# Performance work log

Measured on AMD Instinct MI355X. Metric: run time of the kernel, lower is better.

The kernel has to match this reference:

```python
import jax, jax.numpy as jnp
import numpy as np

COMPRESSION = 2  # max-pool factor along flattened spatial axis for phi and g


def setup_inputs() -> dict:
    key = jax.random.key(0)
    ks = jax.random.split(key, 5)
    B, C, H, W = 4, 64, 96, 96
    Ci = 32  # intermediate_dim = C // 2
    s = 1.0 / np.sqrt(C)
    return {
        "x": jax.random.normal(ks[0], (B, C, H, W), dtype=jnp.float32),
        "w_theta": jax.random.normal(ks[1], (Ci, C), dtype=jnp.float32) * s,
        "b_theta": jnp.zeros((Ci,), dtype=jnp.float32),
        "w_phi": jax.random.normal(ks[2], (Ci, C), dtype=jnp.float32) * s,
        "b_phi": jnp.zeros((Ci,), dtype=jnp.float32),
        "w_g": jax.random.normal(ks[3], (Ci, C), dtype=jnp.float32) * s,
        "b_g": jnp.zeros((Ci,), dtype=jnp.float32),
        "w_out": jax.random.normal(ks[4], (C, Ci), dtype=jnp.float32) * (1.0 / np.sqrt(Ci)),
        "b_out": jnp.zeros((C,), dtype=jnp.float32),
    }


def reference(x, w_theta, b_theta, w_phi, b_phi, w_g, b_g, w_out, b_out):
    B, C, H, W = x.shape
    N = H * W
    xf = x.reshape(B, C, N).transpose(0, 2, 1)            # [B, N, C]
    # 1x1 conv projections == channel matmuls
    theta = xf @ w_theta.T + b_theta                      # [B, N, Ci]
    phi = xf @ w_phi.T + b_phi                            # [B, N, Ci]
    g = xf @ w_g.T + b_g                                  # [B, N, Ci]
    # compression: max-pool (kernel=stride=COMPRESSION) along flattened spatial axis
    Ci = theta.shape[-1]
    phi = phi.reshape(B, N // COMPRESSION, COMPRESSION, Ci).max(axis=2)  # [B, N/c, Ci]
    g = g.reshape(B, N // COMPRESSION, COMPRESSION, Ci).max(axis=2)      # [B, N/c, Ci]
    # embedded-gaussian affinity + softmax
    attn = jax.nn.softmax(jnp.einsum('bnc,bmc->bnm', theta, phi), axis=-1)  # [B, N, N/c]
    y = jnp.einsum('bnm,bmc->bnc', attn, g)               # [B, N, Ci]
    out = y @ w_out.T + b_out                             # [B, N, C]
    out = out.transpose(0, 2, 1).reshape(B, C, H, W)
    return out + x  # residual
```

## Files before the change

### kernel.cpp

```cpp
#include <hip/hip_runtime.h>
#include <hip/hip_bf16.h>


#define NQ 9216
#define MM 4608
#define LOG2E 1.44269504088896340736f

typedef __attribute__((ext_vector_type(8))) short bf16x8;
typedef __attribute__((ext_vector_type(4))) float f32x4;
typedef __attribute__((ext_vector_type(4))) unsigned short u16x4;

static __device__ __forceinline__ unsigned pk2(float a, float b) {
    __hip_bfloat162 h = __float22bfloat162_rn(make_float2(a, b));
    return *reinterpret_cast<unsigned*>(&h);
}

__global__ __launch_bounds__(128, 4) void proj_kernel(
    const float* __restrict__ x,
    const float* __restrict__ wt, const float* __restrict__ bt,
    const float* __restrict__ wp, const float* __restrict__ bp,
    const float* __restrict__ wg, const float* __restrict__ bg,
    unsigned short* __restrict__ theta, unsigned short* __restrict__ phi,
    unsigned short* __restrict__ gT, float* __restrict__ pzero)
{
    __shared__ unsigned short gst[32 * 20];

    const int tid  = threadIdx.x;
    const int wid  = tid >> 6;
    const int lane = tid & 63;
    const int q = lane >> 4;
    const int c = lane & 15;

    {
        const int gs = gridDim.x * blockDim.x;
        float4 z4 = {0.f, 0.f, 0.f, 0.f};
        for (int i = blockIdx.x * blockDim.x + tid; i < 304128; i += gs)
            ((float4*)pzero)[i] = z4;
    }

    const int b     = blockIdx.x / 288;
    const int rem   = blockIdx.x % 288;
    const int n0blk = rem * 32;
    const int n0    = n0blk + wid * 16;

    const float* Wm[3] = {wt, wp, wg};
    const float* Bm[3] = {bt, bp, bg};

    bf16x8 wf[3][2][2];
    float bias[3][2];
#pragma unroll
    for (int p = 0; p < 3; ++p) {
#pragma unroll
        for (int ct = 0; ct < 2; ++ct) {
            bias[p][ct] = Bm[p][ct * 16 + c];
#pragma unroll
            for (int ks = 0; ks < 2; ++ks) {
                const float* wsrc = Wm[p] + (ct * 16 + c) * 64 + ks * 32 + q * 8;
                f32x4 w0 = *(const f32x4*)wsrc;
                f32x4 w1 = *(const f32x4*)(wsrc + 4);
                unsigned* wk = (unsigned*)&wf[p][ct][ks];
                wk[0] = pk2(w0[0], w0[1]); wk[1] = pk2(w0[2], w0[3]);
                wk[2] = pk2(w1[0], w1[1]); wk[3] = pk2(w1[2], w1[3]);
            }
        }
    }

    bf16x8 af[2];
#pragma unroll
    for (int ks = 0; ks < 2; ++ks) {
        unsigned* ap = (unsigned*)&af[ks];
#pragma unroll
        for (int j2 = 0; j2 < 4; ++j2) {
            float x0 = x[(b * 64 + ks * 32 + q * 8 + j2 * 2) * NQ + n0 + c];
            float x1 = x[(b * 64 + ks * 32 + q * 8 + j2 * 2 + 1) * NQ + n0 + c];
            ap[j2] = pk2(x0, x1);
        }
    }

#pragma unroll
    for (int p = 0; p < 3; ++p) {
#pragma unroll
        for (int ct = 0; ct < 2; ++ct) {
            f32x4 acc = {0.f, 0.f, 0.f, 0.f};
            acc = __builtin_amdgcn_mfma_f32_16x16x32_bf16(af[0], wf[p][ct][0], acc, 0, 0, 0);
            acc = __builtin_amdgcn_mfma_f32_16x16x32_bf16(af[1], wf[p][ct][1], acc, 0, 0, 0);
#pragma unroll
            for (int r = 0; r < 4; ++r) acc[r] += bias[p][ct];
            const int ci = ct * 16 + c;
            if (p == 0) {
                unsigned pv0 = pk2(acc[0] * LOG2E, acc[1] * LOG2E);
                unsigned pv1 = pk2(acc[2] * LOG2E, acc[3] * LOG2E);
                theta[(b * NQ + n0 + 4 * q + 0) * 32 + ci] = (unsigned short)pv0;
                theta[(b * NQ + n0 + 4 * q + 1) * 32 + ci] = (unsigned short)(pv0 >> 16);
                theta[(b * NQ + n0 + 4 * q + 2) * 32 + ci] = (unsigned short)pv1;
                theta[(b * NQ + n0 + 4 * q + 3) * 32 + ci] = (unsigned short)(pv1 >> 16);
            } else {
                unsigned pv = pk2(fmaxf(acc[0], acc[1]), fmaxf(acc[2], acc[3]));
                if (p == 1) {
                    const int m0 = (n0 >> 1) + 2 * q;
                    phi[(b * MM + m0) * 32 + ci]     = (unsigned short)pv;
                    phi[(b * MM + m0 + 1) * 32 + ci] = (unsigned short)(pv >> 16);
                } else {
                    *(unsigned int*)(gst + ci * 20 + wid * 8 + 2 * q) = pv;
                }
            }
        }
    }

    __syncthreads();
    {
        const int ci = tid >> 2;
        const int m4 = (tid & 3) * 4;
        u16x4 v = *(const u16x4*)(gst + ci * 20 + m4);
        *(u16x4*)(gT + (b * 32 + ci) * MM + rem * 16 + m4) = v;
    }
}

__global__ __launch_bounds__(128, 3) void attn_kernel(
    const unsigned short* __restrict__ theta, const unsigned short* __restrict__ phi,
    const unsigned short* __restrict__ gT,
    float* __restrict__ pacc, float* __restrict__ plsum)
{
    __shared__ unsigned short pld[2][64 * 64];

    const int tid  = threadIdx.x;
    const int w    = tid >> 6;
    const int lane = tid & 63;
    const int q  = lane >> 4;
    const int c  = lane & 15;
    const int xr = (c & 7) << 3;

    const int ks  = blockIdx.x / 288;
    const int rem = blockIdx.x % 288;
    const int b   = rem / 72;
    const int nb  = (rem % 72) * 128 + w * 64;

    bf16x8 qf[4];
#pragma unroll
    for (int rt = 0; rt < 4; ++rt)
        qf[rt] = *(const bf16x8*)(theta + (b * NQ + nb + rt * 16 + c) * 32 + q * 8);

    bf16x8 onef;
    {
        unsigned v = (c == 0) ? 0x3F803F80u : 0u;
        unsigned* op = (unsigned*)&onef;
        op[0] = v; op[1] = v; op[2] = v; op[3] = v;
    }

    const unsigned short* phiB = phi + (size_t)b * MM * 32;
    const unsigned short* gTB  = gT + (size_t)b * 32 * MM;
    unsigned short* myp = pld[w];

    f32x4 acc[4][2];
    f32x4 lacc[4];
#pragma unroll
    for (int rt = 0; rt < 4; ++rt) {
        lacc[rt] = (f32x4){0.f, 0.f, 0.f, 0.f};
#pragma unroll
        for (int s2 = 0; s2 < 2; ++s2) acc[rt][s2] = (f32x4){0.f, 0.f, 0.f, 0.f};
    }

    const int mt0 = ks * 9;
    bf16x8 kf[4], vf[2][2];

#define LOAD_KF(m0) do {                                                      \
    _Pragma("unroll")                                                         \
    for (int mct = 0; mct < 4; ++mct)                                         \
        kf[mct] = *(const bf16x8*)(phiB + ((m0) + mct * 16 + c) * 32 + q * 8);\
} while (0)

#define LOAD_VF(m0) do {                                                      \
    _Pragma("unroll")                                                         \
    for (int s2 = 0; s2 < 2; ++s2) {                                          \
        _Pragma("unroll")                                                     \
        for (int st = 0; st < 2; ++st)                                        \
            vf[s2][st] = *(const bf16x8*)(gTB + (s2 * 16 + c) * MM + (m0) + st * 32 + q * 8); \
    }                                                                         \
} while (0)

#define S_STEP(rt) do {                                                       \
    _Pragma("unroll")                                                         \
    for (int mct = 0; mct < 4; ++mct) {                                       \
        f32x4 z = {0.f, 0.f, 0.f, 0.f};                                       \
        f32x4 s = __builtin_amdgcn_mfma_f32_16x16x32_bf16(kf[mct], qf[rt], z, 0, 0, 0); \
        uint2 hv = {pk2(__builtin_amdgcn_exp2f(s[0]), __builtin_amdgcn_exp2f(s[1])),    \
                    pk2(__builtin_amdgcn_exp2f(s[2]), __builtin_amdgcn_exp2f(s[3]))};   \
        *(uint2*)(myp + (((rt) * 16 + c) << 6) + ((mct * 16 + 4 * q) ^ xr)) = hv;       \
    }                                                                         \
} while (0)

#define PV_STEP(rt) do {                                                      \
    bf16x8 pf0 = *(const bf16x8*)(myp + (((rt) * 16 + c) << 6) + ((q * 8) ^ xr));       \
    bf16x8 pf1 = *(const bf16x8*)(myp + (((rt) * 16 + c) << 6) + ((32 + q * 8) ^ xr));  \
    __builtin_amdgcn_s_setprio(1);                                            \
    acc[rt][0] = __builtin_amdgcn_mfma_f32_16x16x32_bf16(vf[0][0], pf0, acc[rt][0], 0, 0, 0); \
    acc[rt][1] = __builtin_amdgcn_mfma_f32_16x16x32_bf16(vf[1][0], pf0, acc[rt][1], 0, 0, 0); \
    lacc[rt]   = __builtin_amdgcn_mfma_f32_16x16x32_bf16(onef,     pf0, lacc[rt],   0, 0, 0); \
    acc[rt][0] = __builtin_amdgcn_mfma_f32_16x16x32_bf16(vf[0][1], pf1, acc[rt][0], 0, 0, 0); \
    acc[rt][1] = __builtin_amdgcn_mfma_f32_16x16x32_bf16(vf[1][1], pf1, acc[rt][1], 0, 0, 0); \
    lacc[rt]   = __builtin_amdgcn_mfma_f32_16x16x32_bf16(onef,     pf1, lacc[rt],   0, 0, 0); \
    __builtin_amdgcn_s_setprio(0);                                            \
} while (0)

    LOAD_KF(mt0 * 64);
    LOAD_VF(mt0 * 64);
    S_STEP(0); S_STEP(1); S_STEP(2); S_STEP(3);

    for (int mi = 1; mi < 9; ++mi) {
        const int m0 = (mt0 + mi) * 64;

        LOAD_KF(m0);

        PV_STEP(0);
        PV_STEP(1);
        S_STEP(0);
        PV_STEP(2);
        S_STEP(1);
        PV_STEP(3);

        LOAD_VF(m0);

        S_STEP(2);
        S_STEP(3);
    }

    PV_STEP(0); PV_STEP(1); PV_STEP(2); PV_STEP(3);

#undef LOAD_KF
#undef LOAD_VF
#undef S_STEP
#undef PV_STEP

#pragma unroll
    for (int rt = 0; rt < 4; ++rt)
#pragma unroll
        for (int s2 = 0; s2 < 2; ++s2)
#pragma unroll
            for (int r = 0; r < 4; ++r)
                atomicAdd(&pacc[(size_t)(b * 32 + s2 * 16 + 4 * q + r) * NQ + nb + rt * 16 + c],
                          acc[rt][s2][r]);
    if (lane < 16) {
#pragma unroll
        for (int rt = 0; rt < 4; ++rt)
            atomicAdd(&plsum[(size_t)b * NQ + nb + rt * 16 + lane], lacc[rt][0]);
    }
}

__global__ __launch_bounds__(128, 4) void reduce_kernel(
    const float* __restrict__ pacc, const float* __restrict__ plsum,
    const float* __restrict__ w_out, const float* __restrict__ b_out,
    const float* __restrict__ x, float* __restrict__ out)
{
    __shared__ unsigned short yld[32 * 36];

    const int tid = threadIdx.x;
    const int b   = blockIdx.x / 288;
    const int nb  = (blockIdx.x % 288) * 32;

    {
        const int ci = tid >> 2;
        const int n8 = (tid & 3) * 8;
        const float* pr = pacc + (size_t)(b * 32 + ci) * NQ + nb + n8;
        f32x4 a0 = *(const f32x4*)pr;
        f32x4 a1 = *(const f32x4*)(pr + 4);
        const float* lr = plsum + (size_t)b * NQ + nb + n8;
        f32x4 l0 = *(const f32x4*)lr;
        f32x4 l1 = *(const f32x4*)(lr + 4);
        uint2 v0 = {pk2(a0[0] / l0[0], a0[1] / l0[1]), pk2(a0[2] / l0[2], a0[3] / l0[3])};
        uint2 v1 = {pk2(a1[0] / l1[0], a1[1] / l1[1]), pk2(a1[2] / l1[2], a1[3] / l1[3])};
        *(uint2*)(yld + ci * 36 + n8)     = v0;
        *(uint2*)(yld + ci * 36 + n8 + 4) = v1;
    }
    __syncthreads();

    const int w    = tid >> 6;
    const int lane = tid & 63;
    const int q = lane >> 4;
    const int c = lane & 15;

    bf16x8 wof[4];
#pragma unroll
    for (int ct = 0; ct < 4; ++ct) {
        const float* wsrc = w_out + (ct * 16 + c) * 32 + q * 8;
        f32x4 w0 = *(const f32x4*)wsrc;
        f32x4 w1 = *(const f32x4*)(wsrc + 4);
        unsigned* wk = (unsigned*)&wof[ct];
        wk[0] = pk2(w0[0], w0[1]); wk[1] = pk2(w0[2], w0[3]);
        wk[2] = pk2(w1[0], w1[1]); wk[3] = pk2(w1[2], w1[3]);
    }

    bf16x8 yf;
    {
        unsigned short* yp = (unsigned short*)&yf;
#pragma unroll
        for (int j = 0; j < 8; ++j)
            yp[j] = yld[(q * 8 + j) * 36 + w * 16 + c];
    }

#pragma unroll
    for (int ct = 0; ct < 4; ++ct) {
        f32x4 z = {0.f, 0.f, 0.f, 0.f};
        f32x4 o = __builtin_amdgcn_mfma_f32_16x16x32_bf16(wof[ct], yf, z, 0, 0, 0);
#pragma unroll
        for (int r = 0; r < 4; ++r) {
            const int chn = ct * 16 + 4 * q + r;
            const size_t addr = (size_t)(b * 64 + chn) * NQ + nb + w * 16 + c;
            out[addr] = o[r] + b_out[chn] + x[addr];
        }
    }
}

extern "C" void kernel_launch(void* const* d_in, const int* in_sizes, int n_in,
                              void* d_out, int out_size, void* d_ws, size_t ws_size,
                              hipStream_t stream) {
    const float* x       = (const float*)d_in[0];
    const float* w_theta = (const float*)d_in[1];
    const float* b_theta = (const float*)d_in[2];
    const float* w_phi   = (const float*)d_in[3];
    const float* b_phi   = (const float*)d_in[4];
    const float* w_g     = (const float*)d_in[5];
    const float* b_g     = (const float*)d_in[6];
    const float* w_out   = (const float*)d_in[7];
    const float* b_out   = (const float*)d_in[8];
    float* out = (float*)d_out;

    unsigned short* theta = (unsigned short*)d_ws;
    unsigned short* phi   = theta + 4 * NQ * 32;
    unsigned short* gT    = phi + 4 * MM * 32;
    float* pacc  = (float*)(gT + 4 * 32 * MM);
    float* plsum = pacc + (size_t)4 * 32 * NQ;

    proj_kernel<<<1152, 128, 0, stream>>>(x, w_theta, b_theta, w_phi, b_phi,
                                          w_g, b_g, theta, phi, gT, pacc);
    attn_kernel<<<8 * 288, 128, 0, stream>>>(theta, phi, gT, pacc, plsum);
    reduce_kernel<<<1152, 128, 0, stream>>>(pacc, plsum, w_out, b_out, x, out);
}
```

Before: 143.5 us.

## Shrink attention key tile to 32, split keys 12 ways, sum softmax denominator in VALU

The attention kernel now processes 32-key tiles instead of 64 and splits the key range into 12 chunks instead of 8, launching more blocks with a higher occupancy target. The row-sum of exponentials is accumulated in scalar registers and reduced with cross-lane shuffles, replacing the extra MFMA with a ones vector. The LDS swizzle and buffer shrink to match, and the interleaved S/PV schedule plus setprio hints are dropped in favour of a simpler sequential order. The aim is lower register and LDS pressure and fewer wasted MFMAs, at the cost of more atomic traffic to the partial accumulators and less overlap between the two matmul stages.

```diff
diff --git a/kernel.cpp b/kernel.cpp
--- a/kernel.cpp
+++ b/kernel.cpp
@@ -4,6 +4,8 @@
 
 #define NQ 9216
 #define MM 4608
+#define KS 12
+#define TPW 12
 #define LOG2E 1.44269504088896340736f
 
 typedef __attribute__((ext_vector_type(8))) short bf16x8;
@@ -116,19 +118,19 @@
     }
 }
 
-__global__ __launch_bounds__(128, 3) void attn_kernel(
+__global__ __launch_bounds__(128, 5) void attn_kernel(
     const unsigned short* __restrict__ theta, const unsigned short* __restrict__ phi,
     const unsigned short* __restrict__ gT,
     float* __restrict__ pacc, float* __restrict__ plsum)
 {
-    __shared__ unsigned short pld[2][64 * 64];
+    __shared__ unsigned short pld[2][64 * 32];
 
     const int tid  = threadIdx.x;
     const int w    = tid >> 6;
     const int lane = tid & 63;
     const int q  = lane >> 4;
     const int c  = lane & 15;
-    const int xr = (c & 7) << 3;
+    const int sw = ((c >> 1) & 3) << 3;
 
     const int ks  = blockIdx.x / 288;
     const int rem = blockIdx.x % 288;
@@ -140,88 +142,63 @@
     for (int rt = 0; rt < 4; ++rt)
         qf[rt] = *(const bf16x8*)(theta + (b * NQ + nb + rt * 16 + c) * 32 + q * 8);
 
-    bf16x8 onef;
-    {
-        unsigned v = (c == 0) ? 0x3F803F80u : 0u;
-        unsigned* op = (unsigned*)&onef;
-        op[0] = v; op[1] = v; op[2] = v; op[3] = v;
-    }
-
     const unsigned short* phiB = phi + (size_t)b * MM * 32;
     const unsigned short* gTB  = gT + (size_t)b * 32 * MM;
     unsigned short* myp = pld[w];
 
     f32x4 acc[4][2];
-    f32x4 lacc[4];
+    float lsum[4];
 #pragma unroll
     for (int rt = 0; rt < 4; ++rt) {
-        lacc[rt] = (f32x4){0.f, 0.f, 0.f, 0.f};
+        lsum[rt] = 0.f;
 #pragma unroll
         for (int s2 = 0; s2 < 2; ++s2) acc[rt][s2] = (f32x4){0.f, 0.f, 0.f, 0.f};
     }
 
-    const int mt0 = ks * 9;
-    bf16x8 kf[4], vf[2][2];
+    const int t0 = ks * TPW;
+    bf16x8 kf[2], vf[2];
 
 #define LOAD_KF(m0) do {                                                      \
-    _Pragma("unroll")                                                         \
-    for (int mct = 0; mct < 4; ++mct)                                         \
-        kf[mct] = *(const bf16x8*)(phiB + ((m0) + mct * 16 + c) * 32 + q * 8);\
+    kf[0] = *(const bf16x8*)(phiB + ((m0) + c) * 32 + q * 8);                 \
+    kf[1] = *(const bf16x8*)(phiB + ((m0) + 16 + c) * 32 + q * 8);            \
 } while (0)
 
 #define LOAD_VF(m0) do {                                                      \
-    _Pragma("unroll")                                                         \
-    for (int s2 = 0; s2 < 2; ++s2) {                                          \
-        _Pragma("unroll")                                                     \
-        for (int st = 0; st < 2; ++st)                                        \
-            vf[s2][st] = *(const bf16x8*)(gTB + (s2 * 16 + c) * MM + (m0) + st * 32 + q * 8); \
-    }                                                                         \
+    vf[0] = *(const bf16x8*)(gTB + c * MM + (m0) + q * 8);                    \
+    vf[1] = *(const bf16x8*)(gTB + (16 + c) * MM + (m0) + q * 8);             \
 } while (0)
 
-#define S_STEP(rt) do {                                                       \
-    _Pragma("unroll")                                                         \
-    for (int mct = 0; mct < 4; ++mct) {                                       \
-        f32x4 z = {0.f, 0.f, 0.f, 0.f};                                       \
+#define S_STEP(rt) do {                                                      \
+    _Pragma("unroll")                                                        \
+    for (int mct = 0; mct < 2; ++mct) {                                      \
+        f32x4 z = {0.f, 0.f, 0.f, 0.f};                                      \
         f32x4 s = __builtin_amdgcn_mfma_f32_16x16x32_bf16(kf[mct], qf[rt], z, 0, 0, 0); \
-        uint2 hv = {pk2(__builtin_amdgcn_exp2f(s[0]), __builtin_amdgcn_exp2f(s[1])),    \
-                    pk2(__builtin_amdgcn_exp2f(s[2]), __builtin_amdgcn_exp2f(s[3]))};   \
-        *(uint2*)(myp + (((rt) * 16 + c) << 6) + ((mct * 16 + 4 * q) ^ xr)) = hv;       \
-    }                                                                         \
+        float e0 = __builtin_amdgcn_exp2f(s[0]);                             \
+        float e1 = __builtin_amdgcn_exp2f(s[1]);                             \
+        float e2 = __builtin_amdgcn_exp2f(s[2]);                             \
+        float e3 = __builtin_amdgcn_exp2f(s[3]);                             \
+        lsum[rt] += (e0 + e1) + (e2 + e3);                                   \
+        uint2 hv = {pk2(e0, e1), pk2(e2, e3)};                               \
+        *(uint2*)(myp + (((rt) * 16 + c) << 5) + ((mct * 16 + 4 * q) ^ sw)) = hv; \
+    }                                                                        \
 } while (0)
 
-#define PV_STEP(rt) do {                                                      \
-    bf16x8 pf0 = *(const bf16x8*)(myp + (((rt) * 16 + c) << 6) + ((q * 8) ^ xr));       \
-    bf16x8 pf1 = *(const bf16x8*)(myp + (((rt) * 16 + c) << 6) + ((32 + q * 8) ^ xr));  \
-    __builtin_amdgcn_s_setprio(1);                                            \
-    acc[rt][0] = __builtin_amdgcn_mfma_f32_16x16x32_bf16(vf[0][0], pf0, acc[rt][0], 0, 0, 0); \
-    acc[rt][1] = __builtin_amdgcn_mfma_f32_16x16x32_bf16(vf[1][0], pf0, acc[rt][1], 0, 0, 0); \
-    lacc[rt]   = __builtin_amdgcn_mfma_f32_16x16x32_bf16(onef,     pf0, lacc[rt],   0, 0, 0); \
-    acc[rt][0] = __builtin_amdgcn_mfma_f32_16x16x32_bf16(vf[0][1], pf1, acc[rt][0], 0, 0, 0); \
-    acc[rt][1] = __builtin_amdgcn_mfma_f32_16x16x32_bf16(vf[1][1], pf1, acc[rt][1], 0, 0, 0); \
-    lacc[rt]   = __builtin_amdgcn_mfma_f32_16x16x32_bf16(onef,     pf1, lacc[rt],   0, 0, 0); \
-    __builtin_amdgcn_s_setprio(0);                                            \
+#define PV_STEP(rt) do {                                                     \
+    bf16x8 pf = *(const bf16x8*)(myp + (((rt) * 16 + c) << 5) + ((q * 8) ^ sw)); \
+    acc[rt][0] = __builtin_amdgcn_mfma_f32_16x16x32_bf16(vf[0], pf, acc[rt][0], 0, 0, 0); \
+    acc[rt][1] = __builtin_amdgcn_mfma_f32_16x16x32_bf16(vf[1], pf, acc[rt][1], 0, 0, 0); \
 } while (0)
 
-    LOAD_KF(mt0 * 64);
-    LOAD_VF(mt0 * 64);
+    LOAD_KF(t0 * 32);
+    LOAD_VF(t0 * 32);
     S_STEP(0); S_STEP(1); S_STEP(2); S_STEP(3);
 
-    for (int mi = 1; mi < 9; ++mi) {
-        const int m0 = (mt0 + mi) * 64;
-
+    for (int mi = 1; mi < TPW; ++mi) {
+        const int m0 = (t0 + mi) * 32;
         LOAD_KF(m0);
-
-        PV_STEP(0);
-        PV_STEP(1);
-        S_STEP(0);
-        PV_STEP(2);
-        S_STEP(1);
-        PV_STEP(3);
-
+        PV_STEP(0); PV_STEP(1); PV_STEP(2); PV_STEP(3);
         LOAD_VF(m0);
-
-        S_STEP(2);
-        S_STEP(3);
+        S_STEP(0); S_STEP(1); S_STEP(2); S_STEP(3);
     }
 
     PV_STEP(0); PV_STEP(1); PV_STEP(2); PV_STEP(3);
@@ -239,10 +216,19 @@
             for (int r = 0; r < 4; ++r)
                 atomicAdd(&pacc[(size_t)(b * 32 + s2 * 16 + 4 * q + r) * NQ + nb + rt * 16 + c],
                           acc[rt][s2][r]);
+
+    float lv[4];
+#pragma unroll
+    for (int rt = 0; rt < 4; ++rt) {
+        float v = lsum[rt];
+        v += __shfl_xor(v, 16);
+        v += __shfl_xor(v, 32);
+        lv[rt] = v;
+    }
     if (lane < 16) {
 #pragma unroll
         for (int rt = 0; rt < 4; ++rt)
-            atomicAdd(&plsum[(size_t)b * NQ + nb + rt * 16 + lane], lacc[rt][0]);
+            atomicAdd(&plsum[(size_t)b * NQ + nb + rt * 16 + lane], lv[rt]);
     }
 }
 
@@ -332,6 +318,6 @@
 
     proj_kernel<<<1152, 128, 0, stream>>>(x, w_theta, b_theta, w_phi, b_phi,
                                           w_g, b_g, theta, phi, gT, pacc);
-    attn_kernel<<<8 * 288, 128, 0, stream>>>(theta, phi, gT, pacc, plsum);
+    attn_kernel<<<KS * 288, 128, 0, stream>>>(theta, phi, gT, pacc, plsum);
     reduce_kernel<<<1152, 128, 0, stream>>>(pacc, plsum, w_out, b_out, x, out);
 }
```

Result: slower. 175.2 us (+22.1%).
